# Kernel optimization log

Measured on AMD Instinct MI355X. Metric: run time of the kernel, lower is better.

Reference implementation:

```python
import jax, jax.numpy as jnp
import numpy as np

CONF = 0.3      # confidence threshold (NMS.conf)
IOU = 0.6       # IoU threshold (NMS.iou)
MAX_WH = 4096.0 # class-offset trick for per-class NMS
K = 2048        # max candidates entering NMS (yolov5-style cap)
MAX_DET = 300   # max detections kept per image (fixed output size)


def setup_inputs() -> dict:
    key = jax.random.key(0)
    kxy, kwh, kobj, kcls = jax.random.split(key, 4)
    B, N, NC = 8, 25200, 80
    # realistic raw predictions: xywh in pixel units for a 640x640 image
    xy = jax.random.uniform(kxy, (B, N, 2), minval=0.0, maxval=640.0)
    wh = jax.random.uniform(kwh, (B, N, 2), minval=2.0, maxval=160.0)
    obj = jax.random.uniform(kobj, (B, N, 1))
    cls = jax.random.uniform(kcls, (B, N, NC))
    x = jnp.concatenate([xy, wh, obj, cls], axis=-1)  # [B, N, 5+NC]
    return {"x": x}


def _xywh2xyxy(b):
    xy, half = b[..., :2], b[..., 2:4] * 0.5
    return jnp.concatenate([xy - half, xy + half], axis=-1)


def _pairwise_iou(boxes):  # boxes: [K, 4] xyxy -> [K, K]
    lt = jnp.maximum(boxes[:, None, :2], boxes[None, :, :2])
    rb = jnp.minimum(boxes[:, None, 2:], boxes[None, :, 2:])
    inter = jnp.clip(rb - lt, 0.0).prod(-1)
    area = (boxes[:, 2] - boxes[:, 0]) * (boxes[:, 3] - boxes[:, 1])
    return inter / (area[:, None] + area[None, :] - inter + 1e-9)


def _nms_single(pred):  # pred: [N, 5+NC]
    obj = pred[:, 4]
    cls_conf = pred[:, 5:] * obj[:, None]          # conf = obj * cls prob
    conf = cls_conf.max(-1)
    cls_id = jnp.argmax(cls_conf, -1)
    valid = (obj > CONF) & (conf > CONF)           # candidate + final threshold
    boxes = _xywh2xyxy(pred[:, :4])
    scores = jnp.where(valid, conf, -1.0)
    top_s, idx = jax.lax.top_k(scores, K)          # cap candidates, sorted desc
    boxes_k = boxes[idx]
    cls_k = cls_id[idx]
    valid_k = top_s > 0.0
    # offset boxes by class so NMS is per-class
    shifted = boxes_k + cls_k[:, None].astype(boxes_k.dtype) * MAX_WH
    iou = _pairwise_iou(shifted)                   # [K, K]
    order = jnp.arange(K)

    def body(keep, i):  # greedy suppression in score order
        active = keep[i] & valid_k[i]
        sup = (iou[i] > IOU) & (order > i)
        keep = jnp.where(active, keep & ~sup, keep)
        return keep, None

    keep, _ = jax.lax.scan(body, jnp.ones((K,), bool), order)
    keep = keep & valid_k
    final_s = jnp.where(keep, top_s, -1.0)
    det_s, det_i = jax.lax.top_k(final_s, MAX_DET)
    dets = jnp.concatenate(
        [boxes_k[det_i], top_s[det_i][:, None],
         cls_k[det_i][:, None].astype(boxes_k.dtype)], axis=-1)  # [MAX_DET, 6]
    return dets, det_s > 0.0


def reference(x):
    # returns (dets [B, MAX_DET, 6] = xyxy,conf,cls ; valid mask [B, MAX_DET])
    return jax.vmap(_nms_single)(x)
```

## Files before the change

### kernel.cpp

```cpp
#include <hip/hip_runtime.h>

#define B 8
#define N 25200
#define ROW 85
#define NC 80
#define K 2048
#define MAXDET 300
#define NBUCKET 16384
#define CAND_CAP 4096
#define NCHUNK 32
#define STILE 64
#define CTR_STRIDE 64

__global__ void __launch_bounds__(256)
nms_score_kernel(const float* __restrict__ x,
                 float* __restrict__ scores,
                 int* __restrict__ cls_id,
                 float4* __restrict__ boxes4,
                 unsigned* __restrict__ ready,
                 unsigned* __restrict__ done_ctr) {
    int b = blockIdx.y;
    int i0 = blockIdx.x * STILE;
    if (blockIdx.x == 0 && threadIdx.x == 0) {
        ready[b * CTR_STRIDE] = 0u;
        done_ctr[b * CTR_STRIDE] = 0u;
    }
    int rows = N - i0; if (rows > STILE) rows = STILE;
    __shared__ float lx[STILE * ROW];
    {
        const float4* s4 = (const float4*)(x + ((size_t)b * N + i0) * ROW);
        float4* d4 = (float4*)lx;
        int nv = rows * ROW / 4;
        for (int k = threadIdx.x; k < nv; k += 256) d4[k] = s4[k];
    }
    __syncthreads();
    int g = threadIdx.x >> 2;
    int q = threadIdx.x & 3;
    if (g >= rows) return;
    const float* p = lx + g * ROW;
    float obj = p[4];
    float best = -1e30f;
    int bc = 127;
    if (obj > 0.3f) {
        #pragma unroll
        for (int k = 0; k < 20; ++k) {
            int c = q + 4 * k;
            float v = __fmul_rn(p[5 + c], obj);
            if (v > best) { best = v; bc = c; }
        }
    }
    #pragma unroll
    for (int m = 1; m < 4; m <<= 1) {
        float ov = __shfl_xor(best, m, 64);
        int   oc = __shfl_xor(bc, m, 64);
        if (ov > best || (ov == best && oc < bc)) { best = ov; bc = oc; }
    }
    if (q == 0) {
        int i = i0 + g;
        float score = (obj > 0.3f && best > 0.3f) ? best : -1.0f;
        scores[b * N + i] = score;
        cls_id[b * N + i] = (bc == 127) ? 0 : bc;
        float cx = p[0], cy = p[1], w = p[2], h = p[3];
        float hx = __fmul_rn(w, 0.5f);
        float hy = __fmul_rn(h, 0.5f);
        boxes4[b * N + i] = make_float4(__fsub_rn(cx, hx), __fsub_rn(cy, hy),
                                        __fadd_rn(cx, hx), __fadd_rn(cy, hy));
    }
}

__global__ void __launch_bounds__(1024, 1)
nms_tail_kernel(const float* __restrict__ scores,
                const float4* __restrict__ boxes4,
                const int* __restrict__ cls_id,
                float* __restrict__ top_s,
                float* __restrict__ boxes,
                int* __restrict__ clsk,
                float* __restrict__ shifted,
                float* __restrict__ area,
                unsigned long long* __restrict__ keepbits,
                unsigned long long* __restrict__ gclsmask,
                unsigned* __restrict__ ready,
                unsigned* __restrict__ done_ctr,
                float* __restrict__ out) {
    __shared__ unsigned loff[NBUCKET];
    __shared__ unsigned lcnt16[NBUCKET / 2];
    __shared__ unsigned long long lk[CAND_CAP];
    __shared__ unsigned long long lcm[NC * NCHUNK];
    __shared__ unsigned wsum[16];

    int bid = blockIdx.x;
    int t = threadIdx.x;
    int ln = t & 63, wv = t >> 6;
    unsigned long long below = (ln == 0) ? 0ULL : (~0ULL >> (64 - ln));

    if (bid < B) {
        int b = bid;
        constexpr int NITER = (N + 1023) / 1024;

        if (t < NCHUNK) keepbits[b * NCHUNK + t] = 0ULL;
        {
            uint4 z = {0u, 0u, 0u, 0u};
            uint4* d1 = (uint4*)loff;
            for (int k = t; k < NBUCKET / 4; k += 1024) d1[k] = z;
            uint4* d2 = (uint4*)lcnt16;
            for (int k = t; k < NBUCKET / 8; k += 1024) d2[k] = z;
        }
        for (int k = t; k < CAND_CAP; k += 1024) lk[k] = 0ULL;
        for (int k = t; k < NC * NCHUNK; k += 1024) lcm[k] = 0ULL;
        __syncthreads();

        float sreg[NITER];
        #pragma unroll
        for (int r = 0; r < NITER; ++r) {
            int i = t + r * 1024;
            float s = (i < N) ? scores[b * N + i] : -1.0f;
            sreg[r] = s;
            if (s > 0.0f) {
                int q = (int)(__fmul_rn(s, 16384.0f));
                if (q > NBUCKET - 1) q = NBUCKET - 1;
                atomicAdd(&loff[q], 1u);
            }
        }
        __syncthreads();

        unsigned v[16];
        unsigned A4 = (unsigned)(NBUCKET - 16 - t * 16) / 4;
        {
            uint4 u0 = ((uint4*)loff)[A4 + 0];
            uint4 u1 = ((uint4*)loff)[A4 + 1];
            uint4 u2 = ((uint4*)loff)[A4 + 2];
            uint4 u3 = ((uint4*)loff)[A4 + 3];
            unsigned u[16] = {u0.x,u0.y,u0.z,u0.w, u1.x,u1.y,u1.z,u1.w,
                              u2.x,u2.y,u2.z,u2.w, u3.x,u3.y,u3.z,u3.w};
            #pragma unroll
            for (int k = 0; k < 16; ++k) v[k] = u[15 - k];
        }
        unsigned S = 0;
        #pragma unroll
        for (int k = 0; k < 16; ++k) S += v[k];
        unsigned pref = S;
        #pragma unroll
        for (int o = 1; o < 64; o <<= 1) { unsigned u = __shfl_up(pref, o, 64); if (ln >= o) pref += u; }
        if (ln == 63) wsum[wv] = pref;
        __syncthreads();
        unsigned wbase = 0;
        for (int w = 0; w < wv; ++w) wbase += wsum[w];
        unsigned running = wbase + pref - S;
        {
            unsigned o[16];
            #pragma unroll
            for (int k = 0; k < 16; ++k) { o[15 - k] = running; running += v[k]; }
            ((uint4*)loff)[A4 + 0] = make_uint4(o[0],  o[1],  o[2],  o[3]);
            ((uint4*)loff)[A4 + 1] = make_uint4(o[4],  o[5],  o[6],  o[7]);
            ((uint4*)loff)[A4 + 2] = make_uint4(o[8],  o[9],  o[10], o[11]);
            ((uint4*)loff)[A4 + 3] = make_uint4(o[12], o[13], o[14], o[15]);
        }
        __syncthreads();

        #pragma unroll
        for (int r = 0; r < NITER; ++r) {
            float s = sreg[r];
            if (s > 0.0f) {
                int i = t + r * 1024;
                int q = (int)(__fmul_rn(s, 16384.0f));
                if (q > NBUCKET - 1) q = NBUCKET - 1;
                unsigned start = loff[q];
                if (start < CAND_CAP) {
                    unsigned sh = (q & 1) * 16;
                    unsigned old = atomicAdd(&lcnt16[q >> 1], 1u << sh);
                    unsigned rank = (old >> sh) & 0xFFFFu;
                    unsigned pos = start + rank;
                    if (pos < CAND_CAP) {
                        unsigned long long key =
                            ((unsigned long long)__float_as_uint(s) << 32) | (unsigned)(~i);
                        lk[pos] = key;
                    }
                }
            }
        }
        __syncthreads();

        for (int q = t; q < NBUCKET; q += 1024) {
            unsigned start = loff[q];
            if (start < CAND_CAP) {
                unsigned c = (lcnt16[q >> 1] >> ((q & 1) * 16)) & 0xFFFFu;
                unsigned m = c;
                if (m > CAND_CAP - start) m = CAND_CAP - start;
                if (m >= 2) {
                    for (unsigned a = start + 1; a < start + m; ++a) {
                        unsigned long long kv = lk[a];
                        unsigned p2 = a;
                        while (p2 > start && lk[p2 - 1] < kv) { lk[p2] = lk[p2 - 1]; --p2; }
                        lk[p2] = kv;
                    }
                }
            }
        }
        __syncthreads();

        for (int r = t; r < K; r += 1024) {
            unsigned long long key = lk[r];
            float s;
            int idx;
            float x1, y1, x2, y2;
            int c;
            if (key == 0ULL) {
                s = -1.0f; x1 = y1 = x2 = y2 = 0.0f; c = 0;
            } else {
                s = __uint_as_float((unsigned)(key >> 32));
                idx = (int)(~(unsigned)key);
                float4 bb = boxes4[(size_t)b * N + idx];
                x1 = bb.x; y1 = bb.y; x2 = bb.z; y2 = bb.w;
                c = cls_id[b * N + idx];
                atomicOr(&lcm[c * NCHUNK + (r >> 6)], 1ULL << (r & 63));
            }
            int o = b * K + r;
            top_s[o] = s;
            boxes[o * 4 + 0] = x1; boxes[o * 4 + 1] = y1;
            boxes[o * 4 + 2] = x2; boxes[o * 4 + 3] = y2;
            clsk[o] = c;
            float sh = __fmul_rn((float)c, 4096.0f);
            float sx1 = __fadd_rn(x1, sh), sy1 = __fadd_rn(y1, sh);
            float sx2 = __fadd_rn(x2, sh), sy2 = __fadd_rn(y2, sh);
            shifted[o * 4 + 0] = sx1; shifted[o * 4 + 1] = sy1;
            shifted[o * 4 + 2] = sx2; shifted[o * 4 + 3] = sy2;
            area[o] = __fmul_rn(__fsub_rn(sx2, sx1), __fsub_rn(sy2, sy1));
        }
        __syncthreads();
        for (int k = t; k < NC * NCHUNK; k += 1024)
            gclsmask[(size_t)b * NC * NCHUNK + k] = lcm[k];
        __syncthreads();
        if (t == 0) {
            __threadfence();
            atomicExch(&ready[b * CTR_STRIDE], 1u);
        }
        return;
    }

    int gid = bid - B;
    int b = gid / 5;
    int grp = gid % 5;
    int c = grp * 16 + wv;

    if (t == 0) {
        while (atomicOr(&ready[b * CTR_STRIDE], 0u) == 0u)
            __builtin_amdgcn_s_sleep(8);
        __threadfence();
    }
    __syncthreads();

    const unsigned long long* cm = gclsmask + ((size_t)b * NC + c) * NCHUNK;
    unsigned long long membw = 0ULL;
    int n = 0, r = -1, ch_i = -1, myk = -1;
    unsigned long long mych = 0ULL;
    for (int ch = 0; ch < NCHUNK; ++ch) {
        unsigned long long m = cm[ch];
        if (ln == ch) membw = m;
        int cnt = __popcll(m);
        if (myk < 0 && ln < n + cnt) { mych = m; myk = ln - n; ch_i = ch; }
        n += cnt;
    }
    if (myk >= 0) {
        unsigned long long mm = mych;
        for (int z = 0; z < myk; ++z) mm &= mm - 1;
        r = ch_i * 64 + __builtin_ctzll(mm);
    }

    if (n > 0 && n <= 64) {
        float x1 = 0.f, y1 = 0.f, x2 = 0.f, y2 = 0.f, ar = 0.f;
        if (ln < n) {
            const float* sb = shifted + ((size_t)b * K + r) * 4;
            x1 = sb[0]; y1 = sb[1]; x2 = sb[2]; y2 = sb[3];
            ar = area[b * K + r];
        }
        unsigned long long keepw = (n == 64) ? ~0ULL : ((1ULL << n) - 1ULL);
        for (int i = 0; i < n; ++i) {
            if (!((keepw >> i) & 1ULL)) continue;
            float bx1 = __shfl(x1, i, 64), by1 = __shfl(y1, i, 64);
            float bx2 = __shfl(x2, i, 64), by2 = __shfl(y2, i, 64);
            float ba  = __shfl(ar, i, 64);
            bool cond = false;
            if (ln > i && ln < n) {
                float lx = fmaxf(bx1, x1), ly = fmaxf(by1, y1);
                float rx = fminf(bx2, x2), ry = fminf(by2, y2);
                float w = fmaxf(__fsub_rn(rx, lx), 0.0f);
                float h = fmaxf(__fsub_rn(ry, ly), 0.0f);
                float inter = __fmul_rn(w, h);
                float denom = __fadd_rn(__fsub_rn(__fadd_rn(ba, ar), inter), 1e-9f);
                cond = __fdiv_rn(inter, denom) > 0.6f;
            }
            keepw &= ~__ballot(cond);
        }
        if (ln < n && ((keepw >> ln) & 1ULL))
            atomicOr(&keepbits[b * NCHUNK + (r >> 6)], 1ULL << (r & 63));
    } else if (n > 64) {
        unsigned long long keepw2 = membw;
        for (int i = 0; i < K; ++i) {
            int ch = i >> 6;
            unsigned long long mw = __shfl(membw, ch, 64);
            unsigned long long kw = __shfl(keepw2, ch, 64);
            unsigned long long bi = 1ULL << (i & 63);
            if (!(mw & kw & bi)) continue;
            const float* sbi = shifted + ((size_t)b * K + i) * 4;
            float bx1 = sbi[0], by1 = sbi[1], bx2 = sbi[2], by2 = sbi[3];
            float ba = area[b * K + i];
            for (int c2 = ch; c2 < NCHUNK; ++c2) {
                int j = c2 * 64 + ln;
                unsigned long long mw2 = __shfl(membw, c2, 64);
                bool cond = false;
                if (j > i && ((mw2 >> ln) & 1ULL)) {
                    const float* sbj = shifted + ((size_t)b * K + j) * 4;
                    float x1 = sbj[0], y1 = sbj[1], x2 = sbj[2], y2 = sbj[3];
                    float arj = area[b * K + j];
                    float lx = fmaxf(bx1, x1), ly = fmaxf(by1, y1);
                    float rx = fminf(bx2, x2), ry = fminf(by2, y2);
                    float w = fmaxf(__fsub_rn(rx, lx), 0.0f);
                    float h = fmaxf(__fsub_rn(ry, ly), 0.0f);
                    float inter = __fmul_rn(w, h);
                    float denom = __fadd_rn(__fsub_rn(__fadd_rn(ba, arj), inter), 1e-9f);
                    cond = __fdiv_rn(inter, denom) > 0.6f;
                }
                unsigned long long sup = __ballot(cond);
                if (ln == c2) keepw2 &= ~sup;
            }
        }
        if (ln < NCHUNK && (keepw2 & membw))
            atomicOr(&keepbits[b * NCHUNK + ln], keepw2 & membw);
    }

    __threadfence();
    unsigned old = 0;
    if (ln == 0) old = atomicAdd(&done_ctr[b * CTR_STRIDE], 1u);
    old = (unsigned)__shfl((int)old, 0, 64);
    if (old == NC - 1) {
        __threadfence();
        unsigned long long kw = 0ULL;
        if (ln < NCHUNK) kw = atomicOr(&keepbits[b * NCHUNK + ln], 0ULL);
        int total = 0;
        for (int ch = 0; ch < NCHUNK; ++ch) total += __popcll(__shfl(kw, ch, 64));

        float* dets  = out + (size_t)b * MAXDET * 6;
        float* flags = out + (size_t)B * MAXDET * 6 + (size_t)b * MAXDET;
        int kc = 0, nc2 = 0;
        for (int ch = 0; ch < NCHUNK; ++ch) {
            int i = ch * 64 + ln;
            unsigned long long m = __shfl(kw, ch, 64);
            bool k = ((m >> ln) & 1ULL) != 0ULL;
            int pc = __popcll(m);
            int slot = k ? (kc + __popcll(m & below))
                         : (total + nc2 + __popcll((~m) & below));
            if (slot < MAXDET) {
                int o = b * K + i;
                dets[slot * 6 + 0] = boxes[o * 4 + 0];
                dets[slot * 6 + 1] = boxes[o * 4 + 1];
                dets[slot * 6 + 2] = boxes[o * 4 + 2];
                dets[slot * 6 + 3] = boxes[o * 4 + 3];
                dets[slot * 6 + 4] = top_s[o];
                dets[slot * 6 + 5] = (float)clsk[o];
                flags[slot] = k ? 1.0f : 0.0f;
            }
            kc += pc;
            nc2 += 64 - pc;
        }
    }
}

extern "C" void kernel_launch(void* const* d_in, const int* in_sizes, int n_in,
                              void* d_out, int out_size, void* d_ws, size_t ws_size,
                              hipStream_t stream) {
    const float* x = (const float*)d_in[0];
    float* out = (float*)d_out;

    char* ws = (char*)d_ws;
    size_t off = 0;
    auto alloc = [&](size_t bytes) -> void* {
        void* p = ws + off;
        off += bytes;
        off = (off + 255) & ~(size_t)255;
        return p;
    };

    float*    scores = (float*)    alloc((size_t)B * N * 4);
    int*      cls_id = (int*)      alloc((size_t)B * N * 4);
    float4*   boxes4 = (float4*)   alloc((size_t)B * N * 16);
    float*    top_s  = (float*)    alloc((size_t)B * K * 4);
    float*    boxes  = (float*)    alloc((size_t)B * K * 4 * 4);
    int*      clsk   = (int*)      alloc((size_t)B * K * 4);
    float*    shifted= (float*)    alloc((size_t)B * K * 4 * 4);
    float*    area   = (float*)    alloc((size_t)B * K * 4);
    unsigned long long* keepbits = (unsigned long long*) alloc((size_t)B * NCHUNK * 8);
    unsigned long long* gclsmask = (unsigned long long*) alloc((size_t)B * NC * NCHUNK * 8);
    unsigned* ready    = (unsigned*) alloc((size_t)B * CTR_STRIDE * 4);
    unsigned* done_ctr = (unsigned*) alloc((size_t)B * CTR_STRIDE * 4);
    (void)ws_size;

    nms_score_kernel<<<dim3((N + STILE - 1) / STILE, B), 256, 0, stream>>>(
        x, scores, cls_id, boxes4, ready, done_ctr);
    nms_tail_kernel<<<B + 5 * B, 1024, 0, stream>>>(
        scores, boxes4, cls_id, top_s, boxes, clsk, shifted, area,
        keepbits, gclsmask, ready, done_ctr, out);
}
```

Baseline: 141.9 us.

## Pre-pack per-class candidate boxes in producer block for NMS workers

The producer block now stages shifted boxes and areas in shared memory, which is unioned with the histogram buffers. For each class it writes a compact packed array of up to 64 candidates plus a count to global memory. Per-class NMS workers then read this contiguous pack instead of rescanning the class bitmasks and gathering scattered boxes. Scores are also reloaded from global memory rather than held in a register array, and the occupancy hint on launch bounds is dropped. The cost is extra packing work and a longer serial section in the producer, in exchange for less consumer latency.

```diff
diff --git a/kernel.cpp b/kernel.cpp
--- a/kernel.cpp
+++ b/kernel.cpp
@@ -68,7 +68,7 @@
     }
 }
 
-__global__ void __launch_bounds__(1024, 1)
+__global__ void __launch_bounds__(1024)
 nms_tail_kernel(const float* __restrict__ scores,
                 const float4* __restrict__ boxes4,
                 const int* __restrict__ cls_id,
@@ -79,11 +79,15 @@
                 float* __restrict__ area,
                 unsigned long long* __restrict__ keepbits,
                 unsigned long long* __restrict__ gclsmask,
+                float* __restrict__ ppack,
+                unsigned* __restrict__ pcount,
                 unsigned* __restrict__ ready,
                 unsigned* __restrict__ done_ctr,
                 float* __restrict__ out) {
-    __shared__ unsigned loff[NBUCKET];
-    __shared__ unsigned lcnt16[NBUCKET / 2];
+    __shared__ union {
+        struct { unsigned loff[NBUCKET]; unsigned lcnt16[NBUCKET / 2]; } a;
+        struct { float sx1[K], sy1[K], sx2[K], sy2[K], sar[K]; } b2;
+    } U;
     __shared__ unsigned long long lk[CAND_CAP];
     __shared__ unsigned long long lcm[NC * NCHUNK];
     __shared__ unsigned wsum[16];
@@ -100,25 +104,22 @@
         if (t < NCHUNK) keepbits[b * NCHUNK + t] = 0ULL;
         {
             uint4 z = {0u, 0u, 0u, 0u};
-            uint4* d1 = (uint4*)loff;
-            for (int k = t; k < NBUCKET / 4; k += 1024) d1[k] = z;
-            uint4* d2 = (uint4*)lcnt16;
-            for (int k = t; k < NBUCKET / 8; k += 1024) d2[k] = z;
+            uint4* d1 = (uint4*)&U.a;
+            for (int k = t; k < (NBUCKET + NBUCKET / 2) / 4; k += 1024) d1[k] = z;
         }
         for (int k = t; k < CAND_CAP; k += 1024) lk[k] = 0ULL;
         for (int k = t; k < NC * NCHUNK; k += 1024) lcm[k] = 0ULL;
         __syncthreads();
 
-        float sreg[NITER];
-        #pragma unroll
         for (int r = 0; r < NITER; ++r) {
             int i = t + r * 1024;
-            float s = (i < N) ? scores[b * N + i] : -1.0f;
-            sreg[r] = s;
-            if (s > 0.0f) {
-                int q = (int)(__fmul_rn(s, 16384.0f));
-                if (q > NBUCKET - 1) q = NBUCKET - 1;
-                atomicAdd(&loff[q], 1u);
+            if (i < N) {
+                float s = scores[b * N + i];
+                if (s > 0.0f) {
+                    int q = (int)(__fmul_rn(s, 16384.0f));
+                    if (q > NBUCKET - 1) q = NBUCKET - 1;
+                    atomicAdd(&U.a.loff[q], 1u);
+                }
             }
         }
         __syncthreads();
@@ -126,10 +127,10 @@
         unsigned v[16];
         unsigned A4 = (unsigned)(NBUCKET - 16 - t * 16) / 4;
         {
-            uint4 u0 = ((uint4*)loff)[A4 + 0];
-            uint4 u1 = ((uint4*)loff)[A4 + 1];
-            uint4 u2 = ((uint4*)loff)[A4 + 2];
-            uint4 u3 = ((uint4*)loff)[A4 + 3];
+            uint4 u0 = ((uint4*)U.a.loff)[A4 + 0];
+            uint4 u1 = ((uint4*)U.a.loff)[A4 + 1];
+            uint4 u2 = ((uint4*)U.a.loff)[A4 + 2];
+            uint4 u3 = ((uint4*)U.a.loff)[A4 + 3];
             unsigned u[16] = {u0.x,u0.y,u0.z,u0.w, u1.x,u1.y,u1.z,u1.w,
                               u2.x,u2.y,u2.z,u2.w, u3.x,u3.y,u3.z,u3.w};
             #pragma unroll
@@ -150,30 +151,31 @@
             unsigned o[16];
             #pragma unroll
             for (int k = 0; k < 16; ++k) { o[15 - k] = running; running += v[k]; }
-            ((uint4*)loff)[A4 + 0] = make_uint4(o[0],  o[1],  o[2],  o[3]);
-            ((uint4*)loff)[A4 + 1] = make_uint4(o[4],  o[5],  o[6],  o[7]);
-            ((uint4*)loff)[A4 + 2] = make_uint4(o[8],  o[9],  o[10], o[11]);
-            ((uint4*)loff)[A4 + 3] = make_uint4(o[12], o[13], o[14], o[15]);
-        }
-        __syncthreads();
-
-        #pragma unroll
+            ((uint4*)U.a.loff)[A4 + 0] = make_uint4(o[0],  o[1],  o[2],  o[3]);
+            ((uint4*)U.a.loff)[A4 + 1] = make_uint4(o[4],  o[5],  o[6],  o[7]);
+            ((uint4*)U.a.loff)[A4 + 2] = make_uint4(o[8],  o[9],  o[10], o[11]);
+            ((uint4*)U.a.loff)[A4 + 3] = make_uint4(o[12], o[13], o[14], o[15]);
+        }
+        __syncthreads();
+
         for (int r = 0; r < NITER; ++r) {
-            float s = sreg[r];
-            if (s > 0.0f) {
-                int i = t + r * 1024;
-                int q = (int)(__fmul_rn(s, 16384.0f));
-                if (q > NBUCKET - 1) q = NBUCKET - 1;
-                unsigned start = loff[q];
-                if (start < CAND_CAP) {
-                    unsigned sh = (q & 1) * 16;
-                    unsigned old = atomicAdd(&lcnt16[q >> 1], 1u << sh);
-                    unsigned rank = (old >> sh) & 0xFFFFu;
-                    unsigned pos = start + rank;
-                    if (pos < CAND_CAP) {
-                        unsigned long long key =
-                            ((unsigned long long)__float_as_uint(s) << 32) | (unsigned)(~i);
-                        lk[pos] = key;
+            int i = t + r * 1024;
+            if (i < N) {
+                float s = scores[b * N + i];
+                if (s > 0.0f) {
+                    int q = (int)(__fmul_rn(s, 16384.0f));
+                    if (q > NBUCKET - 1) q = NBUCKET - 1;
+                    unsigned start = U.a.loff[q];
+                    if (start < CAND_CAP) {
+                        unsigned sh = (q & 1) * 16;
+                        unsigned old = atomicAdd(&U.a.lcnt16[q >> 1], 1u << sh);
+                        unsigned rank = (old >> sh) & 0xFFFFu;
+                        unsigned pos = start + rank;
+                        if (pos < CAND_CAP) {
+                            unsigned long long key =
+                                ((unsigned long long)__float_as_uint(s) << 32) | (unsigned)(~i);
+                            lk[pos] = key;
+                        }
                     }
                 }
             }
@@ -181,9 +183,9 @@
         __syncthreads();
 
         for (int q = t; q < NBUCKET; q += 1024) {
-            unsigned start = loff[q];
+            unsigned start = U.a.loff[q];
             if (start < CAND_CAP) {
-                unsigned c = (lcnt16[q >> 1] >> ((q & 1) * 16)) & 0xFFFFu;
+                unsigned c = (U.a.lcnt16[q >> 1] >> ((q & 1) * 16)) & 0xFFFFu;
                 unsigned m = c;
                 if (m > CAND_CAP - start) m = CAND_CAP - start;
                 if (m >= 2) {
@@ -224,9 +226,33 @@
             float sx2 = __fadd_rn(x2, sh), sy2 = __fadd_rn(y2, sh);
             shifted[o * 4 + 0] = sx1; shifted[o * 4 + 1] = sy1;
             shifted[o * 4 + 2] = sx2; shifted[o * 4 + 3] = sy2;
-            area[o] = __fmul_rn(__fsub_rn(sx2, sx1), __fsub_rn(sy2, sy1));
-        }
-        __syncthreads();
+            float ar = __fmul_rn(__fsub_rn(sx2, sx1), __fsub_rn(sy2, sy1));
+            area[o] = ar;
+            U.b2.sx1[r] = sx1; U.b2.sy1[r] = sy1;
+            U.b2.sx2[r] = sx2; U.b2.sy2[r] = sy2;
+            U.b2.sar[r] = ar;
+        }
+        __syncthreads();
+
+        for (int c = wv; c < NC; c += 16) {
+            int n = 0;
+            for (int ch = 0; ch < NCHUNK; ++ch) {
+                unsigned long long m = lcm[c * NCHUNK + ch];
+                if ((m >> ln) & 1ULL) {
+                    int pos = n + __popcll(m & below);
+                    if (pos < 64) {
+                        int r = ch * 64 + ln;
+                        float* pe = ppack + (((size_t)b * NC + c) * 64 + pos) * 6;
+                        pe[0] = U.b2.sx1[r]; pe[1] = U.b2.sy1[r];
+                        pe[2] = U.b2.sx2[r]; pe[3] = U.b2.sy2[r];
+                        pe[4] = U.b2.sar[r];
+                        pe[5] = __uint_as_float((unsigned)r);
+                    }
+                }
+                n += __popcll(m);
+            }
+            if (ln == 0) pcount[b * NC + c] = (unsigned)n;
+        }
         for (int k = t; k < NC * NCHUNK; k += 1024)
             gclsmask[(size_t)b * NC * NCHUNK + k] = lcm[k];
         __syncthreads();
@@ -249,29 +275,15 @@
     }
     __syncthreads();
 
-    const unsigned long long* cm = gclsmask + ((size_t)b * NC + c) * NCHUNK;
-    unsigned long long membw = 0ULL;
-    int n = 0, r = -1, ch_i = -1, myk = -1;
-    unsigned long long mych = 0ULL;
-    for (int ch = 0; ch < NCHUNK; ++ch) {
-        unsigned long long m = cm[ch];
-        if (ln == ch) membw = m;
-        int cnt = __popcll(m);
-        if (myk < 0 && ln < n + cnt) { mych = m; myk = ln - n; ch_i = ch; }
-        n += cnt;
-    }
-    if (myk >= 0) {
-        unsigned long long mm = mych;
-        for (int z = 0; z < myk; ++z) mm &= mm - 1;
-        r = ch_i * 64 + __builtin_ctzll(mm);
-    }
+    int n = (int)pcount[b * NC + c];
 
     if (n > 0 && n <= 64) {
         float x1 = 0.f, y1 = 0.f, x2 = 0.f, y2 = 0.f, ar = 0.f;
+        int r = -1;
         if (ln < n) {
-            const float* sb = shifted + ((size_t)b * K + r) * 4;
-            x1 = sb[0]; y1 = sb[1]; x2 = sb[2]; y2 = sb[3];
-            ar = area[b * K + r];
+            const float* pe = ppack + (((size_t)b * NC + c) * 64 + ln) * 6;
+            x1 = pe[0]; y1 = pe[1]; x2 = pe[2]; y2 = pe[3]; ar = pe[4];
+            r = (int)__float_as_uint(pe[5]);
         }
         unsigned long long keepw = (n == 64) ? ~0ULL : ((1ULL << n) - 1ULL);
         for (int i = 0; i < n; ++i) {
@@ -294,6 +306,8 @@
         if (ln < n && ((keepw >> ln) & 1ULL))
             atomicOr(&keepbits[b * NCHUNK + (r >> 6)], 1ULL << (r & 63));
     } else if (n > 64) {
+        const unsigned long long* cm = gclsmask + ((size_t)b * NC + c) * NCHUNK;
+        unsigned long long membw = (ln < NCHUNK) ? cm[ln] : 0ULL;
         unsigned long long keepw2 = membw;
         for (int i = 0; i < K; ++i) {
             int ch = i >> 6;
@@ -390,6 +404,8 @@
     float*    area   = (float*)    alloc((size_t)B * K * 4);
     unsigned long long* keepbits = (unsigned long long*) alloc((size_t)B * NCHUNK * 8);
     unsigned long long* gclsmask = (unsigned long long*) alloc((size_t)B * NC * NCHUNK * 8);
+    float*    ppack  = (float*)    alloc((size_t)B * NC * 64 * 6 * 4);
+    unsigned* pcount = (unsigned*) alloc((size_t)B * NC * 4);
     unsigned* ready    = (unsigned*) alloc((size_t)B * CTR_STRIDE * 4);
     unsigned* done_ctr = (unsigned*) alloc((size_t)B * CTR_STRIDE * 4);
     (void)ws_size;
@@ -398,5 +414,5 @@
         x, scores, cls_id, boxes4, ready, done_ctr);
     nms_tail_kernel<<<B + 5 * B, 1024, 0, stream>>>(
         scores, boxes4, cls_id, top_s, boxes, clsk, shifted, area,
-        keepbits, gclsmask, ready, done_ctr, out);
+        keepbits, gclsmask, ppack, pcount, ready, done_ctr, out);
 }
```

After: 170.6 us. +20.2%, slower.

## Pass sorted keys instead of gathered box arrays between sort and NMS blocks

Applied to the files above, without the earlier changes.

The sort block no longer gathers boxes, scores, classes, shifted boxes and areas into global arrays or writes per-class masks. It writes only the sorted 64-bit keys. Each class-NMS block loads the keys into shared memory, rebuilds the class masks locally with shared atomics, and gathers boxes from boxes4 by index on demand, recomputing the shifted boxes and areas. Shared memory is overlaid through a union to fit the new buffers. This shortens the serial work in the sort block and cuts global traffic, but every NMS block now repeats the mask build and does indirect gathers inside the suppression loop.

```diff
diff --git a/kernel.cpp b/kernel.cpp
--- a/kernel.cpp
+++ b/kernel.cpp
@@ -72,20 +72,22 @@
 nms_tail_kernel(const float* __restrict__ scores,
                 const float4* __restrict__ boxes4,
                 const int* __restrict__ cls_id,
-                float* __restrict__ top_s,
-                float* __restrict__ boxes,
-                int* __restrict__ clsk,
-                float* __restrict__ shifted,
-                float* __restrict__ area,
+                unsigned long long* __restrict__ gkeys,
                 unsigned long long* __restrict__ keepbits,
-                unsigned long long* __restrict__ gclsmask,
                 unsigned* __restrict__ ready,
                 unsigned* __restrict__ done_ctr,
                 float* __restrict__ out) {
-    __shared__ unsigned loff[NBUCKET];
-    __shared__ unsigned lcnt16[NBUCKET / 2];
-    __shared__ unsigned long long lk[CAND_CAP];
-    __shared__ unsigned long long lcm[NC * NCHUNK];
+    __shared__ union {
+        struct {
+            unsigned loff[NBUCKET];
+            unsigned lcnt16[NBUCKET / 2];
+            unsigned long long lk[CAND_CAP];
+        } s;
+        struct {
+            unsigned long long keys[K];
+            unsigned long long lcm[NC * NCHUNK];
+        } c;
+    } U;
     __shared__ unsigned wsum[16];
 
     int bid = blockIdx.x;
@@ -100,13 +102,10 @@
         if (t < NCHUNK) keepbits[b * NCHUNK + t] = 0ULL;
         {
             uint4 z = {0u, 0u, 0u, 0u};
-            uint4* d1 = (uint4*)loff;
-            for (int k = t; k < NBUCKET / 4; k += 1024) d1[k] = z;
-            uint4* d2 = (uint4*)lcnt16;
-            for (int k = t; k < NBUCKET / 8; k += 1024) d2[k] = z;
-        }
-        for (int k = t; k < CAND_CAP; k += 1024) lk[k] = 0ULL;
-        for (int k = t; k < NC * NCHUNK; k += 1024) lcm[k] = 0ULL;
+            uint4* d1 = (uint4*)U.s.loff;
+            for (int k = t; k < (NBUCKET + NBUCKET / 2) / 4; k += 1024) d1[k] = z;
+        }
+        for (int k = t; k < CAND_CAP; k += 1024) U.s.lk[k] = 0ULL;
         __syncthreads();
 
         float sreg[NITER];
@@ -118,7 +117,7 @@
             if (s > 0.0f) {
                 int q = (int)(__fmul_rn(s, 16384.0f));
                 if (q > NBUCKET - 1) q = NBUCKET - 1;
-                atomicAdd(&loff[q], 1u);
+                atomicAdd(&U.s.loff[q], 1u);
             }
         }
         __syncthreads();
@@ -126,10 +125,10 @@
         unsigned v[16];
         unsigned A4 = (unsigned)(NBUCKET - 16 - t * 16) / 4;
         {
-            uint4 u0 = ((uint4*)loff)[A4 + 0];
-            uint4 u1 = ((uint4*)loff)[A4 + 1];
-            uint4 u2 = ((uint4*)loff)[A4 + 2];
-            uint4 u3 = ((uint4*)loff)[A4 + 3];
+            uint4 u0 = ((uint4*)U.s.loff)[A4 + 0];
+            uint4 u1 = ((uint4*)U.s.loff)[A4 + 1];
+            uint4 u2 = ((uint4*)U.s.loff)[A4 + 2];
+            uint4 u3 = ((uint4*)U.s.loff)[A4 + 3];
             unsigned u[16] = {u0.x,u0.y,u0.z,u0.w, u1.x,u1.y,u1.z,u1.w,
                               u2.x,u2.y,u2.z,u2.w, u3.x,u3.y,u3.z,u3.w};
             #pragma unroll
@@ -150,10 +149,10 @@
             unsigned o[16];
             #pragma unroll
             for (int k = 0; k < 16; ++k) { o[15 - k] = running; running += v[k]; }
-            ((uint4*)loff)[A4 + 0] = make_uint4(o[0],  o[1],  o[2],  o[3]);
-            ((uint4*)loff)[A4 + 1] = make_uint4(o[4],  o[5],  o[6],  o[7]);
-            ((uint4*)loff)[A4 + 2] = make_uint4(o[8],  o[9],  o[10], o[11]);
-            ((uint4*)loff)[A4 + 3] = make_uint4(o[12], o[13], o[14], o[15]);
+            ((uint4*)U.s.loff)[A4 + 0] = make_uint4(o[0],  o[1],  o[2],  o[3]);
+            ((uint4*)U.s.loff)[A4 + 1] = make_uint4(o[4],  o[5],  o[6],  o[7]);
+            ((uint4*)U.s.loff)[A4 + 2] = make_uint4(o[8],  o[9],  o[10], o[11]);
+            ((uint4*)U.s.loff)[A4 + 3] = make_uint4(o[12], o[13], o[14], o[15]);
         }
         __syncthreads();
 
@@ -164,16 +163,16 @@
                 int i = t + r * 1024;
                 int q = (int)(__fmul_rn(s, 16384.0f));
                 if (q > NBUCKET - 1) q = NBUCKET - 1;
-                unsigned start = loff[q];
+                unsigned start = U.s.loff[q];
                 if (start < CAND_CAP) {
                     unsigned sh = (q & 1) * 16;
-                    unsigned old = atomicAdd(&lcnt16[q >> 1], 1u << sh);
+                    unsigned old = atomicAdd(&U.s.lcnt16[q >> 1], 1u << sh);
                     unsigned rank = (old >> sh) & 0xFFFFu;
                     unsigned pos = start + rank;
                     if (pos < CAND_CAP) {
                         unsigned long long key =
                             ((unsigned long long)__float_as_uint(s) << 32) | (unsigned)(~i);
-                        lk[pos] = key;
+                        U.s.lk[pos] = key;
                     }
                 }
             }
@@ -181,54 +180,25 @@
         __syncthreads();
 
         for (int q = t; q < NBUCKET; q += 1024) {
-            unsigned start = loff[q];
+            unsigned start = U.s.loff[q];
             if (start < CAND_CAP) {
-                unsigned c = (lcnt16[q >> 1] >> ((q & 1) * 16)) & 0xFFFFu;
+                unsigned c = (U.s.lcnt16[q >> 1] >> ((q & 1) * 16)) & 0xFFFFu;
                 unsigned m = c;
                 if (m > CAND_CAP - start) m = CAND_CAP - start;
                 if (m >= 2) {
                     for (unsigned a = start + 1; a < start + m; ++a) {
-                        unsigned long long kv = lk[a];
+                        unsigned long long kv = U.s.lk[a];
                         unsigned p2 = a;
-                        while (p2 > start && lk[p2 - 1] < kv) { lk[p2] = lk[p2 - 1]; --p2; }
-                        lk[p2] = kv;
+                        while (p2 > start && U.s.lk[p2 - 1] < kv) { U.s.lk[p2] = U.s.lk[p2 - 1]; --p2; }
+                        U.s.lk[p2] = kv;
                     }
                 }
             }
         }
         __syncthreads();
 
-        for (int r = t; r < K; r += 1024) {
-            unsigned long long key = lk[r];
-            float s;
-            int idx;
-            float x1, y1, x2, y2;
-            int c;
-            if (key == 0ULL) {
-                s = -1.0f; x1 = y1 = x2 = y2 = 0.0f; c = 0;
-            } else {
-                s = __uint_as_float((unsigned)(key >> 32));
-                idx = (int)(~(unsigned)key);
-                float4 bb = boxes4[(size_t)b * N + idx];
-                x1 = bb.x; y1 = bb.y; x2 = bb.z; y2 = bb.w;
-                c = cls_id[b * N + idx];
-                atomicOr(&lcm[c * NCHUNK + (r >> 6)], 1ULL << (r & 63));
-            }
-            int o = b * K + r;
-            top_s[o] = s;
-            boxes[o * 4 + 0] = x1; boxes[o * 4 + 1] = y1;
-            boxes[o * 4 + 2] = x2; boxes[o * 4 + 3] = y2;
-            clsk[o] = c;
-            float sh = __fmul_rn((float)c, 4096.0f);
-            float sx1 = __fadd_rn(x1, sh), sy1 = __fadd_rn(y1, sh);
-            float sx2 = __fadd_rn(x2, sh), sy2 = __fadd_rn(y2, sh);
-            shifted[o * 4 + 0] = sx1; shifted[o * 4 + 1] = sy1;
-            shifted[o * 4 + 2] = sx2; shifted[o * 4 + 3] = sy2;
-            area[o] = __fmul_rn(__fsub_rn(sx2, sx1), __fsub_rn(sy2, sy1));
-        }
-        __syncthreads();
-        for (int k = t; k < NC * NCHUNK; k += 1024)
-            gclsmask[(size_t)b * NC * NCHUNK + k] = lcm[k];
+        for (int r = t; r < K; r += 1024)
+            gkeys[(size_t)b * K + r] = U.s.lk[r];
         __syncthreads();
         if (t == 0) {
             __threadfence();
@@ -249,13 +219,24 @@
     }
     __syncthreads();
 
-    const unsigned long long* cm = gclsmask + ((size_t)b * NC + c) * NCHUNK;
-    unsigned long long membw = 0ULL;
+    for (int r = t; r < K; r += 1024) U.c.keys[r] = gkeys[(size_t)b * K + r];
+    for (int k = t; k < NC * NCHUNK; k += 1024) U.c.lcm[k] = 0ULL;
+    __syncthreads();
+
+    for (int r = t; r < K; r += 1024) {
+        unsigned long long key = U.c.keys[r];
+        if (key != 0ULL) {
+            int idx = (int)(~(unsigned)key);
+            int cc = cls_id[b * N + idx];
+            atomicOr(&U.c.lcm[cc * NCHUNK + (r >> 6)], 1ULL << (r & 63));
+        }
+    }
+    __syncthreads();
+
     int n = 0, r = -1, ch_i = -1, myk = -1;
     unsigned long long mych = 0ULL;
     for (int ch = 0; ch < NCHUNK; ++ch) {
-        unsigned long long m = cm[ch];
-        if (ln == ch) membw = m;
+        unsigned long long m = U.c.lcm[c * NCHUNK + ch];
         int cnt = __popcll(m);
         if (myk < 0 && ln < n + cnt) { mych = m; myk = ln - n; ch_i = ch; }
         n += cnt;
@@ -263,15 +244,20 @@
     if (myk >= 0) {
         unsigned long long mm = mych;
         for (int z = 0; z < myk; ++z) mm &= mm - 1;
-        r = ch_i * 64 + __builtin_ctzll(mm);
-    }
+        r = ch_i * 64 + (int)__builtin_ctzll(mm);
+    }
+
+    float shf = __fmul_rn((float)c, 4096.0f);
 
     if (n > 0 && n <= 64) {
         float x1 = 0.f, y1 = 0.f, x2 = 0.f, y2 = 0.f, ar = 0.f;
         if (ln < n) {
-            const float* sb = shifted + ((size_t)b * K + r) * 4;
-            x1 = sb[0]; y1 = sb[1]; x2 = sb[2]; y2 = sb[3];
-            ar = area[b * K + r];
+            unsigned long long key = U.c.keys[r];
+            int idx = (int)(~(unsigned)key);
+            float4 bb = boxes4[(size_t)b * N + idx];
+            x1 = __fadd_rn(bb.x, shf); y1 = __fadd_rn(bb.y, shf);
+            x2 = __fadd_rn(bb.z, shf); y2 = __fadd_rn(bb.w, shf);
+            ar = __fmul_rn(__fsub_rn(x2, x1), __fsub_rn(y2, y1));
         }
         unsigned long long keepw = (n == 64) ? ~0ULL : ((1ULL << n) - 1ULL);
         for (int i = 0; i < n; ++i) {
@@ -294,6 +280,7 @@
         if (ln < n && ((keepw >> ln) & 1ULL))
             atomicOr(&keepbits[b * NCHUNK + (r >> 6)], 1ULL << (r & 63));
     } else if (n > 64) {
+        unsigned long long membw = (ln < NCHUNK) ? U.c.lcm[c * NCHUNK + ln] : 0ULL;
         unsigned long long keepw2 = membw;
         for (int i = 0; i < K; ++i) {
             int ch = i >> 6;
@@ -301,17 +288,23 @@
             unsigned long long kw = __shfl(keepw2, ch, 64);
             unsigned long long bi = 1ULL << (i & 63);
             if (!(mw & kw & bi)) continue;
-            const float* sbi = shifted + ((size_t)b * K + i) * 4;
-            float bx1 = sbi[0], by1 = sbi[1], bx2 = sbi[2], by2 = sbi[3];
-            float ba = area[b * K + i];
+            unsigned long long keyi = U.c.keys[i];
+            int idxi = (int)(~(unsigned)keyi);
+            float4 bi4 = boxes4[(size_t)b * N + idxi];
+            float bx1 = __fadd_rn(bi4.x, shf), by1 = __fadd_rn(bi4.y, shf);
+            float bx2 = __fadd_rn(bi4.z, shf), by2 = __fadd_rn(bi4.w, shf);
+            float ba = __fmul_rn(__fsub_rn(bx2, bx1), __fsub_rn(by2, by1));
             for (int c2 = ch; c2 < NCHUNK; ++c2) {
                 int j = c2 * 64 + ln;
                 unsigned long long mw2 = __shfl(membw, c2, 64);
                 bool cond = false;
                 if (j > i && ((mw2 >> ln) & 1ULL)) {
-                    const float* sbj = shifted + ((size_t)b * K + j) * 4;
-                    float x1 = sbj[0], y1 = sbj[1], x2 = sbj[2], y2 = sbj[3];
-                    float arj = area[b * K + j];
+                    unsigned long long keyj = U.c.keys[j];
+                    int idxj = (int)(~(unsigned)keyj);
+                    float4 bj4 = boxes4[(size_t)b * N + idxj];
+                    float x1 = __fadd_rn(bj4.x, shf), y1 = __fadd_rn(bj4.y, shf);
+                    float x2 = __fadd_rn(bj4.z, shf), y2 = __fadd_rn(bj4.w, shf);
+                    float arj = __fmul_rn(__fsub_rn(x2, x1), __fsub_rn(y2, y1));
                     float lx = fmaxf(bx1, x1), ly = fmaxf(by1, y1);
                     float rx = fminf(bx2, x2), ry = fminf(by2, y2);
                     float w = fmaxf(__fsub_rn(rx, lx), 0.0f);
@@ -350,13 +343,23 @@
             int slot = k ? (kc + __popcll(m & below))
                          : (total + nc2 + __popcll((~m) & below));
             if (slot < MAXDET) {
-                int o = b * K + i;
-                dets[slot * 6 + 0] = boxes[o * 4 + 0];
-                dets[slot * 6 + 1] = boxes[o * 4 + 1];
-                dets[slot * 6 + 2] = boxes[o * 4 + 2];
-                dets[slot * 6 + 3] = boxes[o * 4 + 3];
-                dets[slot * 6 + 4] = top_s[o];
-                dets[slot * 6 + 5] = (float)clsk[o];
+                unsigned long long key = U.c.keys[i];
+                float s, ox1, oy1, ox2, oy2; int oc;
+                if (key == 0ULL) {
+                    s = -1.0f; ox1 = oy1 = ox2 = oy2 = 0.0f; oc = 0;
+                } else {
+                    s = __uint_as_float((unsigned)(key >> 32));
+                    int idx = (int)(~(unsigned)key);
+                    float4 bb = boxes4[(size_t)b * N + idx];
+                    ox1 = bb.x; oy1 = bb.y; ox2 = bb.z; oy2 = bb.w;
+                    oc = cls_id[b * N + idx];
+                }
+                dets[slot * 6 + 0] = ox1;
+                dets[slot * 6 + 1] = oy1;
+                dets[slot * 6 + 2] = ox2;
+                dets[slot * 6 + 3] = oy2;
+                dets[slot * 6 + 4] = s;
+                dets[slot * 6 + 5] = (float)oc;
                 flags[slot] = k ? 1.0f : 0.0f;
             }
             kc += pc;
@@ -383,13 +386,8 @@
     float*    scores = (float*)    alloc((size_t)B * N * 4);
     int*      cls_id = (int*)      alloc((size_t)B * N * 4);
     float4*   boxes4 = (float4*)   alloc((size_t)B * N * 16);
-    float*    top_s  = (float*)    alloc((size_t)B * K * 4);
-    float*    boxes  = (float*)    alloc((size_t)B * K * 4 * 4);
-    int*      clsk   = (int*)      alloc((size_t)B * K * 4);
-    float*    shifted= (float*)    alloc((size_t)B * K * 4 * 4);
-    float*    area   = (float*)    alloc((size_t)B * K * 4);
+    unsigned long long* gkeys    = (unsigned long long*) alloc((size_t)B * K * 8);
     unsigned long long* keepbits = (unsigned long long*) alloc((size_t)B * NCHUNK * 8);
-    unsigned long long* gclsmask = (unsigned long long*) alloc((size_t)B * NC * NCHUNK * 8);
     unsigned* ready    = (unsigned*) alloc((size_t)B * CTR_STRIDE * 4);
     unsigned* done_ctr = (unsigned*) alloc((size_t)B * CTR_STRIDE * 4);
     (void)ws_size;
@@ -397,6 +395,5 @@
     nms_score_kernel<<<dim3((N + STILE - 1) / STILE, B), 256, 0, stream>>>(
         x, scores, cls_id, boxes4, ready, done_ctr);
     nms_tail_kernel<<<B + 5 * B, 1024, 0, stream>>>(
-        scores, boxes4, cls_id, top_s, boxes, clsk, shifted, area,
-        keepbits, gclsmask, ready, done_ctr, out);
+        scores, boxes4, cls_id, gkeys, keepbits, ready, done_ctr, out);
 }
```

New measurement: 141.3 us. Within noise of the previous version (-0.4%).
